# Performance work log

Measured on AMD Instinct MI355X. Metric: run time of the kernel, lower is better.

## Reference

```python
import jax, jax.numpy as jnp
import numpy as np

# Dims: B=batch, H=query heads, HKV=kv heads, T=query len, S=cache/key len, Dh=head dim
B, H, HKV, T, S, Dh = 2, 32, 8, 1024, 2048, 128
THRESH = 0.000488  # keep keys whose mean attention (over heads and queries) exceeds this


def setup_inputs() -> dict:
    key = jax.random.key(0)
    k1, k2, k3 = jax.random.split(key, 3)
    # attn_w emulates post-softmax attention probabilities: rows sum to 1 over key axis
    attn_w = jax.random.uniform(k1, (B, H, T, S), dtype=jnp.float32)
    attn_w = attn_w / attn_w.sum(axis=-1, keepdims=True)
    v = jax.random.normal(k2, (B, HKV, S, Dh), dtype=jnp.float32)
    w_o = jax.random.normal(k3, (H * Dh, H * Dh), dtype=jnp.float32) * 0.02  # o_proj weight (no bias, Mistral)
    return {"attn_w": attn_w, "v": v, "w_o": w_o}


def reference(attn_w, v, w_o):
    # keep = attn_w.mean(dim=(1,2)) > thresh  -> [B, S]
    keep = attn_w.mean(axis=(1, 2)) > THRESH
    pruned_weights = attn_w * keep[:, None, None, :].astype(attn_w.dtype)  # [B,H,T,S]
    # repeat_kv: [B,HKV,S,Dh] -> [B,H,S,Dh] via repeat_interleave on head axis
    groups = attn_w.shape[1] // v.shape[1]
    v_full = jnp.repeat(v, groups, axis=1)
    new_ctx = jnp.einsum('bhts,bhsd->bhtd', pruned_weights, v_full)  # [B,H,T,Dh]
    Bn, Hn, Tn, Dn = new_ctx.shape
    new_ctx = new_ctx.transpose(0, 2, 1, 3).reshape(Bn, Tn, Hn * Dn)  # [B,T,H*Dh]
    out = new_ctx @ w_o.T  # o_proj
    return (out, pruned_weights)
```

## Files before the change

kernel.cpp:

```cpp
#include <hip/hip_runtime.h>
#include <hip/hip_bf16.h>

#define B_ 2
#define H_ 32
#define HKV_ 8
#define T_ 1024
#define S_ 2048
#define DH_ 128
#define HD_ 4096
#define NROW_ 32768
#define THRESH_D 0.000488

typedef __attribute__((ext_vector_type(4))) float f32x4;
typedef __attribute__((ext_vector_type(8))) short bf16x8;

#define SCHED0() __builtin_amdgcn_sched_barrier(0)

__device__ __forceinline__ void gload_lds16(const void* g, void* l) {
  __builtin_amdgcn_global_load_lds(
      (const __attribute__((address_space(1))) void*)g,
      (__attribute__((address_space(3))) void*)l, 16, 0, 0);
}


__global__ void reduce_keep_k(const double* __restrict__ partial,
                              float* __restrict__ keep) {
  __shared__ double sh[4][64];
  int b = blockIdx.x >> 5;
  int s0 = (blockIdx.x & 31) * 64;
  int w = threadIdx.x >> 6, l = threadIdx.x & 63;
  const double* p = partial + (size_t)b * 256 * S_ + s0 + l;
  double sum = 0.0;
  #pragma unroll 8
  for (int y = 0; y < 64; ++y) sum += p[(size_t)(w * 64 + y) * S_];
  sh[w][l] = sum;
  __syncthreads();
  if (w == 0) {
    double t = (sh[0][l] + sh[1][l]) + (sh[2][l] + sh[3][l]);
    keep[b * S_ + s0 + l] = (t * (1.0 / 32768.0) > THRESH_D) ? 1.0f : 0.0f;
  }
}

__global__ void convert_wo_k(const float* __restrict__ w,
                             __hip_bfloat16* __restrict__ wb) {
  size_t idx = ((size_t)blockIdx.x * 256 + threadIdx.x) * 8;
  int n = (int)(idx >> 12);
  int k0 = (int)(idx & (HD_ - 1));
  float4 x = *(const float4*)(w + idx);
  float4 y = *(const float4*)(w + idx + 4);
  union { bf16x8 v8; __hip_bfloat16 h[8]; } u;
  u.h[0] = __float2bfloat16(x.x); u.h[1] = __float2bfloat16(x.y);
  u.h[2] = __float2bfloat16(x.z); u.h[3] = __float2bfloat16(x.w);
  u.h[4] = __float2bfloat16(y.x); u.h[5] = __float2bfloat16(y.y);
  u.h[6] = __float2bfloat16(y.z); u.h[7] = __float2bfloat16(y.w);
  int ksw = (k0 & ~63) | ((k0 ^ ((n & 7) << 3)) & 63);
  *(bf16x8*)(wb + (size_t)n * HD_ + ksw) = u.v8;
}

#define BK2 64
#define NS2 64

__global__ __launch_bounds__(512) void gemm2_k(
    const __hip_bfloat16* __restrict__ Actx,
    const __hip_bfloat16* __restrict__ Bw,
    float* __restrict__ out) {
  __shared__ __align__(16) __hip_bfloat16 As[2][128 * BK2];
  __shared__ __align__(16) __hip_bfloat16 Bs[2][128 * BK2];
  int tid = threadIdx.x;
  int lg = ((blockIdx.x & 7) << 6) | (blockIdx.x >> 3);
  int n0 = (lg >> 4) * 128;
  int m0 = (lg & 15) * 128;
  const __hip_bfloat16* Ap = Actx + (size_t)m0 * HD_;
  const __hip_bfloat16* Bp = Bw + (size_t)n0 * HD_;
  int wave = tid >> 6, lane = tid & 63;
  int l16 = lane & 15, lk = lane >> 4;

  f32x4 acc[8];
  f32x4 z = {0.f, 0.f, 0.f, 0.f};
  #pragma unroll
  for (int n = 0; n < 8; ++n) acc[n] = z;

  auto issue = [&](int ks, int buf) {
    const __hip_bfloat16* ga = Ap + (size_t)(tid >> 3) * HD_ + ks * BK2 + (tid & 7) * 8;
    const __hip_bfloat16* gb = Bp + (size_t)(tid >> 3) * HD_ + ks * BK2 + (tid & 7) * 8;
    char* la = (char*)&As[buf][0] + tid * 16;
    char* lb = (char*)&Bs[buf][0] + tid * 16;
    gload_lds16(ga, la);
    gload_lds16(ga + (size_t)64 * HD_, la + 8192);
    gload_lds16(gb, lb);
    gload_lds16(gb + (size_t)64 * HD_, lb + 8192);
  };

  auto mfmaStep = [&](int buf) {
    char* ab = (char*)&As[buf][0];
    char* bb = (char*)&Bs[buf][0];
    #pragma unroll
    for (int kk = 0; kk < 2; ++kk) {
      int kb = kk * 64 + lk * 16;
      int ar = wave * 16 + l16;
      bf16x8 af = *(const bf16x8*)(ab + (ar * 128 + (kb ^ ((ar & 7) << 4))));
      #pragma unroll
      for (int n = 0; n < 8; ++n) {
        int br = n * 16 + l16;
        bf16x8 bf = *(const bf16x8*)(bb + (br * 128 + (kb ^ ((br & 7) << 4))));
        acc[n] = __builtin_amdgcn_mfma_f32_16x16x32_bf16(af, bf, acc[n], 0, 0, 0);
      }
    }
  };

  issue(0, 0);
  for (int ks = 0; ks < NS2; ++ks) {
    int cur = ks & 1;
    if (ks + 1 < NS2) issue(ks + 1, cur ^ 1);
    SCHED0();
    if (ks + 1 < NS2) {
      asm volatile("s_waitcnt vmcnt(4) lgkmcnt(0)" ::: "memory");
    } else {
      asm volatile("s_waitcnt vmcnt(0) lgkmcnt(0)" ::: "memory");
    }
    SCHED0();
    __builtin_amdgcn_s_barrier();
    SCHED0();
    mfmaStep(cur);
    SCHED0();
    __builtin_amdgcn_s_barrier();
    SCHED0();
  }

  #pragma unroll
  for (int n = 0; n < 8; ++n)
    #pragma unroll
    for (int r = 0; r < 4; ++r) {
      int row = m0 + wave * 16 + lk * 4 + r;
      int col = n0 + n * 16 + l16;
      out[(size_t)row * HD_ + col] = acc[n][r];
    }
}


__global__ __launch_bounds__(256) void colsumA_k(
    const float* __restrict__ attn, double* __restrict__ partial,
    __hip_bfloat16* __restrict__ abf) {
  int tid = threadIdx.x;
  int b = blockIdx.z, y = blockIdx.y;
  int s = blockIdx.x * 1024 + tid * 4;
  const float* base = attn + (size_t)(b * NROW_ + y * 128) * S_ + s;
  __hip_bfloat16* ob = abf + (size_t)(b * NROW_ + y * 128) * S_;
  double a0 = 0.0, a1 = 0.0, a2 = 0.0, a3 = 0.0;
  #pragma unroll 2
  for (int r = 0; r < 128; ++r) {
    f32x4 vv = *(const f32x4*)(base + (size_t)r * S_);
    a0 += vv.x; a1 += vv.y; a2 += vv.z; a3 += vv.w;
    int ssw = (s & ~63) | ((s ^ ((r & 7) << 3)) & 63);
    union { ushort4 u4; __hip_bfloat16 h[4]; } u;
    u.h[0] = __float2bfloat16(vv.x); u.h[1] = __float2bfloat16(vv.y);
    u.h[2] = __float2bfloat16(vv.z); u.h[3] = __float2bfloat16(vv.w);
    *(ushort4*)(ob + (size_t)r * S_ + ssw) = u.u4;
  }
  double* o = partial + (size_t)(b * 256 + y) * S_ + s;
  o[0] = a0; o[1] = a1; o[2] = a2; o[3] = a3;
}

__global__ void convert_vA_k(const float* __restrict__ v,
                             const float* __restrict__ keep,
                             __hip_bfloat16* __restrict__ vt) {
  __shared__ float tile[32][33];
  int bh = blockIdx.z;
  int b = bh >> 3;
  int s0 = blockIdx.x * 32, d0 = blockIdx.y * 32;
  const float* vp = v + (size_t)bh * (S_ * DH_);
  __hip_bfloat16* vtp = vt + (size_t)bh * (S_ * DH_);
  int tx = threadIdx.x, ty = threadIdx.y;
  for (int i = 0; i < 32; i += 8)
    tile[ty + i][tx] = vp[(size_t)(s0 + ty + i) * DH_ + d0 + tx];
  __syncthreads();
  int s = s0 + tx;
  float kv = keep[b * S_ + s];
  for (int i = 0; i < 32; i += 8) {
    int d = d0 + ty + i;
    int ssw = (s & ~63) | ((s ^ ((d & 7) << 3)) & 63);
    vtp[(size_t)d * S_ + ssw] = __float2bfloat16(tile[tx][ty + i] * kv);
  }
}

#define BK1 64
#define NS1 32

__global__ __launch_bounds__(512, 4) void prune_gemm1A_k(
    const __hip_bfloat16* __restrict__ abf, const float* __restrict__ keep,
    const __hip_bfloat16* __restrict__ vt, float* __restrict__ pruned,
    __hip_bfloat16* __restrict__ ctx) {
  __shared__ __align__(16) __hip_bfloat16 As[2][128 * BK1];
  __shared__ __align__(16) __hip_bfloat16 Bs[2][128 * BK1];
  __shared__ __align__(16) float ksh[S_];

  int tid = threadIdx.x;
  int lg = ((blockIdx.x & 7) << 6) | (blockIdx.x >> 3);
  int bh = lg >> 3;
  int t0 = (lg & 7) * 128;
  int b = bh >> 5, h = bh & 31, hkv = h >> 2;
  int rot = (lg * 17) & 31;
  const __hip_bfloat16* Ab = abf + ((size_t)bh * T_ + t0) * S_;
  float* P = pruned + ((size_t)bh * T_ + t0) * S_;
  const __hip_bfloat16* Bv = vt + (size_t)(b * HKV_ + hkv) * (DH_ * S_);
  const float* kp = keep + b * S_;

  int wave = tid >> 6, lane = tid & 63;
  int l16 = lane & 15, lk = lane >> 4;

  f32x4 acc[8];
  f32x4 z = {0.f, 0.f, 0.f, 0.f};
  #pragma unroll
  for (int n = 0; n < 8; ++n) acc[n] = z;

  auto col = [&](int j) { return (j + rot) & 31; };

  auto issueA = [&](int cks, int buf) {
    const __hip_bfloat16* g0 = Ab + (size_t)(tid >> 3) * S_ + cks * BK1 + (tid & 7) * 8;
    char* la = (char*)&As[buf][0] + tid * 16;
    gload_lds16(g0, la);
    gload_lds16(g0 + (size_t)64 * S_, la + 8192);
  };

  auto issueB = [&](int cks, int buf) {
    const __hip_bfloat16* g0 = Bv + (size_t)(tid >> 3) * S_ + cks * BK1 + (tid & 7) * 8;
    char* lb = (char*)&Bs[buf][0] + tid * 16;
    gload_lds16(g0, lb);
    gload_lds16(g0 + (size_t)64 * S_, lb + 8192);
  };

  auto mfmaStep = [&](int buf) {
    char* ab = (char*)&As[buf][0];
    char* bb = (char*)&Bs[buf][0];
    #pragma unroll
    for (int kk = 0; kk < 2; ++kk) {
      int kb = kk * 64 + lk * 16;
      int ar = wave * 16 + l16;
      bf16x8 af = *(const bf16x8*)(ab + (ar * 128 + (kb ^ ((ar & 7) << 4))));
      #pragma unroll
      for (int n = 0; n < 8; ++n) {
        int br = n * 16 + l16;
        bf16x8 bf = *(const bf16x8*)(bb + (br * 128 + (kb ^ ((br & 7) << 4))));
        acc[n] = __builtin_amdgcn_mfma_f32_16x16x32_bf16(af, bf, acc[n], 0, 0, 0);
      }
    }
  };

  auto prunedWrite = [&](int cks, int buf) {
    char* ab = (char*)&As[buf][0];
    union { bf16x8 v; unsigned int d[4]; } u0, u1;
    u0.v = *(const bf16x8*)(ab + tid * 16);
    u1.v = *(const bf16x8*)(ab + tid * 16 + 8192);
    int row0 = tid >> 3;
    int scol = cks * BK1 + (((tid & 7) * 8) ^ ((row0 & 7) << 3));
    f32x4 k0 = *(const f32x4*)&ksh[scol];
    f32x4 k1 = *(const f32x4*)&ksh[scol + 4];
    f32x4 p00, p01, p10, p11;
    p00.x = __uint_as_float(u0.d[0] << 16) * k0.x;
    p00.y = __uint_as_float(u0.d[0] & 0xFFFF0000u) * k0.y;
    p00.z = __uint_as_float(u0.d[1] << 16) * k0.z;
    p00.w = __uint_as_float(u0.d[1] & 0xFFFF0000u) * k0.w;
    p01.x = __uint_as_float(u0.d[2] << 16) * k1.x;
    p01.y = __uint_as_float(u0.d[2] & 0xFFFF0000u) * k1.y;
    p01.z = __uint_as_float(u0.d[3] << 16) * k1.z;
    p01.w = __uint_as_float(u0.d[3] & 0xFFFF0000u) * k1.w;
    p10.x = __uint_as_float(u1.d[0] << 16) * k0.x;
    p10.y = __uint_as_float(u1.d[0] & 0xFFFF0000u) * k0.y;
    p10.z = __uint_as_float(u1.d[1] << 16) * k0.z;
    p10.w = __uint_as_float(u1.d[1] & 0xFFFF0000u) * k0.w;
    p11.x = __uint_as_float(u1.d[2] << 16) * k1.x;
    p11.y = __uint_as_float(u1.d[2] & 0xFFFF0000u) * k1.y;
    p11.z = __uint_as_float(u1.d[3] << 16) * k1.z;
    p11.w = __uint_as_float(u1.d[3] & 0xFFFF0000u) * k1.w;
    float* gp0 = P + (size_t)row0 * S_ + scol;
    float* gp1 = P + (size_t)(row0 + 64) * S_ + scol;
    *(f32x4*)gp0 = p00; *(f32x4*)(gp0 + 4) = p01;
    *(f32x4*)gp1 = p10; *(f32x4*)(gp1 + 4) = p11;
  };

  gload_lds16(kp + tid * 4, (char*)ksh + tid * 16);
  issueA(col(0), 0);
  issueB(col(0), 0);
  SCHED0();
  asm volatile("s_waitcnt vmcnt(4)" ::: "memory");
  SCHED0();
  __builtin_amdgcn_s_barrier();
  SCHED0();

  for (int ks = 0; ks < NS1; ++ks) {
    int cur = ks & 1;
    if (ks + 1 < NS1) {
      issueA(col(ks + 1), cur ^ 1);
      issueB(col(ks + 1), cur ^ 1);
    }
    SCHED0();
    if (ks == 0 || ks == NS1 - 1) {
      asm volatile("s_waitcnt vmcnt(4) lgkmcnt(0)" ::: "memory");
    } else {
      asm volatile("s_waitcnt vmcnt(8) lgkmcnt(0)" ::: "memory");
    }
    SCHED0();
    __builtin_amdgcn_s_barrier();
    SCHED0();
    mfmaStep(cur);
    prunedWrite(col(ks), cur);
    SCHED0();
    __builtin_amdgcn_s_barrier();
    SCHED0();
  }

  #pragma unroll
  for (int n = 0; n < 8; ++n)
    #pragma unroll
    for (int r = 0; r < 4; ++r) {
      int trow = t0 + wave * 16 + lk * 4 + r;
      int rowm = b * T_ + trow;
      int kcol = h * DH_ + n * 16 + l16;
      int ksw = (kcol & ~63) | ((kcol ^ ((rowm & 7) << 3)) & 63);
      ctx[(size_t)rowm * HD_ + ksw] = __float2bfloat16(acc[n][r]);
    }
}


__global__ __launch_bounds__(256) void colsumB_k(
    const float* __restrict__ attn, double* __restrict__ partial) {
  int tid = threadIdx.x;
  int b = blockIdx.z, y = blockIdx.y;
  int s = blockIdx.x * 1024 + tid * 4;
  const float* base = attn + (size_t)(b * NROW_ + y * 128) * S_ + s;
  double a0 = 0.0, a1 = 0.0, a2 = 0.0, a3 = 0.0;
  for (int r = 0; r < 128; ++r) {
    f32x4 vv = *(const f32x4*)(base + (size_t)r * S_);
    a0 += vv.x; a1 += vv.y; a2 += vv.z; a3 += vv.w;
  }
  double* o = partial + (size_t)(b * 256 + y) * S_ + s;
  o[0] = a0; o[1] = a1; o[2] = a2; o[3] = a3;
}

__global__ void convert_vB_k(const float* __restrict__ v,
                             __hip_bfloat16* __restrict__ vt) {
  __shared__ float tile[32][33];
  int bh = blockIdx.z;
  int s0 = blockIdx.x * 32, d0 = blockIdx.y * 32;
  const float* vp = v + (size_t)bh * (S_ * DH_);
  __hip_bfloat16* vtp = vt + (size_t)bh * (S_ * DH_);
  int tx = threadIdx.x, ty = threadIdx.y;
  for (int i = 0; i < 32; i += 8)
    tile[ty + i][tx] = vp[(size_t)(s0 + ty + i) * DH_ + d0 + tx];
  __syncthreads();
  int s = s0 + tx;
  for (int i = 0; i < 32; i += 8) {
    int d = d0 + ty + i;
    int ssw = (s & ~63) | ((s ^ ((d & 7) << 3)) & 63);
    vtp[(size_t)d * S_ + ssw] = __float2bfloat16(tile[tx][ty + i]);
  }
}

__global__ __launch_bounds__(512, 4) void prune_gemm1B_k(
    const float* __restrict__ attn, const float* __restrict__ keep,
    const __hip_bfloat16* __restrict__ vt, float* __restrict__ pruned,
    __hip_bfloat16* __restrict__ ctx) {
  __shared__ __align__(16) __hip_bfloat16 As[2][128 * BK1];
  __shared__ __align__(16) __hip_bfloat16 Bs[2][128 * BK1];
  __shared__ __align__(16) float ksh[S_];

  int tid = threadIdx.x;
  int lg = ((blockIdx.x & 7) << 6) | (blockIdx.x >> 3);
  int bh = lg >> 3;
  int t0 = (lg & 7) * 128;
  int b = bh >> 5, h = bh & 31, hkv = h >> 2;
  int rot = (lg * 17) & 31;
  const float* A = attn + ((size_t)bh * T_ + t0) * S_;
  float* P = pruned + ((size_t)bh * T_ + t0) * S_;
  const __hip_bfloat16* Bv = vt + (size_t)(b * HKV_ + hkv) * (DH_ * S_);
  const float* kp = keep + b * S_;

  int arow = tid >> 2;
  int acol = (tid & 3) * 16;
  int wave = tid >> 6, lane = tid & 63;
  int l16 = lane & 15, lk = lane >> 4;

  f32x4 acc[8];
  f32x4 z = {0.f, 0.f, 0.f, 0.f};
  #pragma unroll
  for (int n = 0; n < 8; ++n) acc[n] = z;

  f32x4 areg0[4], areg1[4];

  auto col = [&](int j) { return (j + rot) & 31; };

  auto issueA = [&](int cks, f32x4* bank) {
    const float* ga = A + (size_t)arow * S_ + cks * BK1 + acol;
    #pragma unroll
    for (int j = 0; j < 4; ++j) bank[j] = *(const f32x4*)(ga + j * 4);
  };

  auto issueB = [&](int cks, int buf) {
    const __hip_bfloat16* g0 = Bv + (size_t)(tid >> 3) * S_ + cks * BK1 + (tid & 7) * 8;
    char* lb = (char*)&Bs[buf][0] + tid * 16;
    gload_lds16(g0, lb);
    gload_lds16(g0 + (size_t)64 * S_, lb + 8192);
  };

  auto stageA = [&](int cks, int buf, const f32x4* bank) {
    f32x4 p[4];
    #pragma unroll
    for (int j = 0; j < 4; ++j) {
      f32x4 kv = *(const f32x4*)&ksh[cks * BK1 + acol + j * 4];
      p[j] = bank[j] * kv;
    }
    float* gp = P + (size_t)arow * S_ + cks * BK1 + acol;
    #pragma unroll
    for (int j = 0; j < 4; ++j) *(f32x4*)(gp + j * 4) = p[j];
    union { bf16x8 v8; __hip_bfloat16 h[8]; } u0, u1;
    const float* pf = (const float*)&p[0];
    #pragma unroll
    for (int j = 0; j < 8; ++j) u0.h[j] = __float2bfloat16(pf[j]);
    #pragma unroll
    for (int j = 0; j < 8; ++j) u1.h[j] = __float2bfloat16(pf[8 + j]);
    char* ab = (char*)&As[buf][0];
    int base0 = arow * 128 + acol * 2;
    int sw = (arow & 7) << 4;
    *(bf16x8*)(ab + (base0 ^ sw)) = u0.v8;
    *(bf16x8*)(ab + ((base0 + 16) ^ sw)) = u1.v8;
  };

  auto mfmaStep = [&](int buf) {
    char* ab = (char*)&As[buf][0];
    char* bb = (char*)&Bs[buf][0];
    #pragma unroll
    for (int kk = 0; kk < 2; ++kk) {
      int kb = kk * 64 + lk * 16;
      int ar = wave * 16 + l16;
      bf16x8 af = *(const bf16x8*)(ab + (ar * 128 + (kb ^ ((ar & 7) << 4))));
      #pragma unroll
      for (int n = 0; n < 8; ++n) {
        int br = n * 16 + l16;
        bf16x8 bf = *(const bf16x8*)(bb + (br * 128 + (kb ^ ((br & 7) << 4))));
        acc[n] = __builtin_amdgcn_mfma_f32_16x16x32_bf16(af, bf, acc[n], 0, 0, 0);
      }
    }
  };

  gload_lds16(kp + tid * 4, (char*)ksh + tid * 16);
  issueB(col(0), 0);
  issueA(col(0), areg0);
  SCHED0();
  asm volatile("s_waitcnt vmcnt(6)" ::: "memory");
  SCHED0();
  __builtin_amdgcn_s_barrier();
  SCHED0();
  issueA(col(1), areg1);
  stageA(col(0), 0, areg0);

  for (int ks = 0; ks < NS1; ks += 2) {
    {
      int cur = 0;
      if (ks + 1 < NS1) issueB(col(ks + 1), 1);
      if (ks + 2 < NS1) issueA(col(ks + 2), areg0);
      if (ks + 1 < NS1) stageA(col(ks + 1), 1, areg1);
      SCHED0();
      if (ks + 2 < NS1)      { asm volatile("s_waitcnt vmcnt(18) lgkmcnt(0)" ::: "memory"); }
      else if (ks + 1 < NS1) { asm volatile("s_waitcnt vmcnt(14) lgkmcnt(0)" ::: "memory"); }
      else                   { asm volatile("s_waitcnt vmcnt(4) lgkmcnt(0)" ::: "memory"); }
      SCHED0();
      __builtin_amdgcn_s_barrier();
      SCHED0();
      mfmaStep(cur);
      SCHED0();
      __builtin_amdgcn_s_barrier();
      SCHED0();
    }
    {
      int ko = ks + 1;
      int cur = 1;
      if (ko + 1 < NS1) issueB(col(ko + 1), 0);
      if (ko + 2 < NS1) issueA(col(ko + 2), areg1);
      if (ko + 1 < NS1) stageA(col(ko + 1), 0, areg0);
      SCHED0();
      if (ko + 2 < NS1)      { asm volatile("s_waitcnt vmcnt(18) lgkmcnt(0)" ::: "memory"); }
      else if (ko + 1 < NS1) { asm volatile("s_waitcnt vmcnt(14) lgkmcnt(0)" ::: "memory"); }
      else                   { asm volatile("s_waitcnt vmcnt(4) lgkmcnt(0)" ::: "memory"); }
      SCHED0();
      __builtin_amdgcn_s_barrier();
      SCHED0();
      mfmaStep(cur);
      SCHED0();
      __builtin_amdgcn_s_barrier();
      SCHED0();
    }
  }

  #pragma unroll
  for (int n = 0; n < 8; ++n)
    #pragma unroll
    for (int r = 0; r < 4; ++r) {
      int trow = t0 + wave * 16 + lk * 4 + r;
      int rowm = b * T_ + trow;
      int kcol = h * DH_ + n * 16 + l16;
      int ksw = (kcol & ~63) | ((kcol ^ ((rowm & 7) << 3)) & 63);
      ctx[(size_t)rowm * HD_ + ksw] = __float2bfloat16(acc[n][r]);
    }
}


extern "C" void kernel_launch(void* const* d_in, const int* in_sizes, int n_in,
                              void* d_out, int out_size, void* d_ws, size_t ws_size,
                              hipStream_t stream) {
  const float* attn = (const float*)d_in[0];
  const float* v = (const float*)d_in[1];
  const float* w_o = (const float*)d_in[2];
  float* out = (float*)d_out;
  float* pruned = out + (size_t)B_ * T_ * HD_;

  char* ws = (char*)d_ws;
  size_t off = 0;
  double* partial = (double*)(ws + off); off += (size_t)B_ * 256 * S_ * 8;
  float* keep = (float*)(ws + off);      off += (size_t)B_ * S_ * 4;
  __hip_bfloat16* vt = (__hip_bfloat16*)(ws + off);
  off += (size_t)B_ * HKV_ * DH_ * S_ * 2;
  __hip_bfloat16* wo = (__hip_bfloat16*)(ws + off);
  off += (size_t)HD_ * HD_ * 2;
  __hip_bfloat16* ctx = (__hip_bfloat16*)(ws + off);
  off += (size_t)B_ * T_ * HD_ * 2;
  __hip_bfloat16* abf = (__hip_bfloat16*)(ws + off);
  size_t need_abf = off + (size_t)B_ * NROW_ * S_ * 2;

  bool bigws = (ws_size >= need_abf);

  if (bigws) {
    colsumA_k<<<dim3(2, 256, B_), 256, 0, stream>>>(attn, partial, abf);
    reduce_keep_k<<<dim3(64), 256, 0, stream>>>(partial, keep);
    convert_vA_k<<<dim3(S_ / 32, DH_ / 32, B_ * HKV_), dim3(32, 8), 0, stream>>>(v, keep, vt);
    convert_wo_k<<<dim3((HD_ * HD_) / (256 * 8)), 256, 0, stream>>>(w_o, wo);
    prune_gemm1A_k<<<dim3(512), 512, 0, stream>>>(abf, keep, vt, pruned, ctx);
  } else {
    colsumB_k<<<dim3(2, 256, B_), 256, 0, stream>>>(attn, partial);
    reduce_keep_k<<<dim3(64), 256, 0, stream>>>(partial, keep);
    convert_vB_k<<<dim3(S_ / 32, DH_ / 32, B_ * HKV_), dim3(32, 8), 0, stream>>>(v, vt);
    convert_wo_k<<<dim3((HD_ * HD_) / (256 * 8)), 256, 0, stream>>>(w_o, wo);
    prune_gemm1B_k<<<dim3(512), 512, 0, stream>>>(attn, keep, vt, pruned, ctx);
  }
  gemm2_k<<<dim3(512), 512, 0, stream>>>(ctx, wo, out);

  (void)in_sizes; (void)n_in; (void)out_size; (void)ws_size;
}
```

Measured before the change: 454.2 us.

## Merge keep-reduction with w_o conversion and rotate colsum row order

Merges the keep-mask reduction and the w_o fp32-to-bf16 conversion into one kernel launch, with the first 64 blocks doing the reduction and the rest converting weights. This removes one launch and lets the two small jobs overlap. The column-sum kernels now start their 128-row loop at a per-block rotated offset, meant to spread concurrent reads across memory channels. In gemm1A the pruned-weight write is moved ahead of the MFMA step so its stores can overlap the math.

```diff
diff --git a/kernel.cpp b/kernel.cpp
--- a/kernel.cpp
+++ b/kernel.cpp
@@ -23,39 +23,41 @@
 }
 
 
-__global__ void reduce_keep_k(const double* __restrict__ partial,
-                              float* __restrict__ keep) {
+__global__ void reduce_wo_k(const double* __restrict__ partial,
+                            float* __restrict__ keep,
+                            const float* __restrict__ w,
+                            __hip_bfloat16* __restrict__ wb) {
   __shared__ double sh[4][64];
-  int b = blockIdx.x >> 5;
-  int s0 = (blockIdx.x & 31) * 64;
-  int w = threadIdx.x >> 6, l = threadIdx.x & 63;
-  const double* p = partial + (size_t)b * 256 * S_ + s0 + l;
-  double sum = 0.0;
-  #pragma unroll 8
-  for (int y = 0; y < 64; ++y) sum += p[(size_t)(w * 64 + y) * S_];
-  sh[w][l] = sum;
-  __syncthreads();
-  if (w == 0) {
-    double t = (sh[0][l] + sh[1][l]) + (sh[2][l] + sh[3][l]);
-    keep[b * S_ + s0 + l] = (t * (1.0 / 32768.0) > THRESH_D) ? 1.0f : 0.0f;
-  }
-}
-
-__global__ void convert_wo_k(const float* __restrict__ w,
-                             __hip_bfloat16* __restrict__ wb) {
-  size_t idx = ((size_t)blockIdx.x * 256 + threadIdx.x) * 8;
-  int n = (int)(idx >> 12);
-  int k0 = (int)(idx & (HD_ - 1));
-  float4 x = *(const float4*)(w + idx);
-  float4 y = *(const float4*)(w + idx + 4);
-  union { bf16x8 v8; __hip_bfloat16 h[8]; } u;
-  u.h[0] = __float2bfloat16(x.x); u.h[1] = __float2bfloat16(x.y);
-  u.h[2] = __float2bfloat16(x.z); u.h[3] = __float2bfloat16(x.w);
-  u.h[4] = __float2bfloat16(y.x); u.h[5] = __float2bfloat16(y.y);
-  u.h[6] = __float2bfloat16(y.z); u.h[7] = __float2bfloat16(y.w);
-  int ksw = (k0 & ~63) | ((k0 ^ ((n & 7) << 3)) & 63);
-  *(bf16x8*)(wb + (size_t)n * HD_ + ksw) = u.v8;
-}
+  if (blockIdx.x < 64) {
+    int b = blockIdx.x >> 5;
+    int s0 = (blockIdx.x & 31) * 64;
+    int wv = threadIdx.x >> 6, l = threadIdx.x & 63;
+    const double* p = partial + (size_t)b * 256 * S_ + s0 + l;
+    double sum = 0.0;
+    #pragma unroll 8
+    for (int y = 0; y < 64; ++y) sum += p[(size_t)(wv * 64 + y) * S_];
+    sh[wv][l] = sum;
+    __syncthreads();
+    if (wv == 0) {
+      double t = (sh[0][l] + sh[1][l]) + (sh[2][l] + sh[3][l]);
+      keep[b * S_ + s0 + l] = (t * (1.0 / 32768.0) > THRESH_D) ? 1.0f : 0.0f;
+    }
+  } else {
+    size_t idx = ((size_t)(blockIdx.x - 64) * 256 + threadIdx.x) * 8;
+    int n = (int)(idx >> 12);
+    int k0 = (int)(idx & (HD_ - 1));
+    float4 x = *(const float4*)(w + idx);
+    float4 y = *(const float4*)(w + idx + 4);
+    union { bf16x8 v8; __hip_bfloat16 h[8]; } u;
+    u.h[0] = __float2bfloat16(x.x); u.h[1] = __float2bfloat16(x.y);
+    u.h[2] = __float2bfloat16(x.z); u.h[3] = __float2bfloat16(x.w);
+    u.h[4] = __float2bfloat16(y.x); u.h[5] = __float2bfloat16(y.y);
+    u.h[6] = __float2bfloat16(y.z); u.h[7] = __float2bfloat16(y.w);
+    int ksw = (k0 & ~63) | ((k0 ^ ((n & 7) << 3)) & 63);
+    *(bf16x8*)(wb + (size_t)n * HD_ + ksw) = u.v8;
+  }
+}
+
 
 #define BK2 64
 #define NS2 64
@@ -146,9 +148,11 @@
   int s = blockIdx.x * 1024 + tid * 4;
   const float* base = attn + (size_t)(b * NROW_ + y * 128) * S_ + s;
   __hip_bfloat16* ob = abf + (size_t)(b * NROW_ + y * 128) * S_;
+  int rot = (y * 37 + b * 11 + blockIdx.x * 53) & 127;
   double a0 = 0.0, a1 = 0.0, a2 = 0.0, a3 = 0.0;
   #pragma unroll 2
-  for (int r = 0; r < 128; ++r) {
+  for (int i = 0; i < 128; ++i) {
+    int r = (i + rot) & 127;
     f32x4 vv = *(const f32x4*)(base + (size_t)r * S_);
     a0 += vv.x; a1 += vv.y; a2 += vv.z; a3 += vv.w;
     int ssw = (s & ~63) | ((s ^ ((r & 7) << 3)) & 63);
@@ -302,8 +306,8 @@
     SCHED0();
     __builtin_amdgcn_s_barrier();
     SCHED0();
+    prunedWrite(col(ks), cur);
     mfmaStep(cur);
-    prunedWrite(col(ks), cur);
     SCHED0();
     __builtin_amdgcn_s_barrier();
     SCHED0();
@@ -328,8 +332,11 @@
   int b = blockIdx.z, y = blockIdx.y;
   int s = blockIdx.x * 1024 + tid * 4;
   const float* base = attn + (size_t)(b * NROW_ + y * 128) * S_ + s;
+  int rot = (y * 37 + b * 11 + blockIdx.x * 53) & 127;
   double a0 = 0.0, a1 = 0.0, a2 = 0.0, a3 = 0.0;
-  for (int r = 0; r < 128; ++r) {
+  #pragma unroll 2
+  for (int i = 0; i < 128; ++i) {
+    int r = (i + rot) & 127;
     f32x4 vv = *(const f32x4*)(base + (size_t)r * S_);
     a0 += vv.x; a1 += vv.y; a2 += vv.z; a3 += vv.w;
   }
@@ -455,7 +462,6 @@
 
   for (int ks = 0; ks < NS1; ks += 2) {
     {
-      int cur = 0;
       if (ks + 1 < NS1) issueB(col(ks + 1), 1);
       if (ks + 2 < NS1) issueA(col(ks + 2), areg0);
       if (ks + 1 < NS1) stageA(col(ks + 1), 1, areg1);
@@ -466,14 +472,13 @@
       SCHED0();
       __builtin_amdgcn_s_barrier();
       SCHED0();
-      mfmaStep(cur);
+      mfmaStep(0);
       SCHED0();
       __builtin_amdgcn_s_barrier();
       SCHED0();
     }
     {
       int ko = ks + 1;
-      int cur = 1;
       if (ko + 1 < NS1) issueB(col(ko + 1), 0);
       if (ko + 2 < NS1) issueA(col(ko + 2), areg1);
       if (ko + 1 < NS1) stageA(col(ko + 1), 0, areg0);
@@ -484,7 +489,7 @@
       SCHED0();
       __builtin_amdgcn_s_barrier();
       SCHED0();
-      mfmaStep(cur);
+      mfmaStep(1);
       SCHED0();
       __builtin_amdgcn_s_barrier();
       SCHED0();
@@ -527,18 +532,17 @@
   size_t need_abf = off + (size_t)B_ * NROW_ * S_ * 2;
 
   bool bigws = (ws_size >= need_abf);
+  int wo_grid = 64 + (HD_ * HD_) / (256 * 8);
 
   if (bigws) {
     colsumA_k<<<dim3(2, 256, B_), 256, 0, stream>>>(attn, partial, abf);
-    reduce_keep_k<<<dim3(64), 256, 0, stream>>>(partial, keep);
+    reduce_wo_k<<<dim3(wo_grid), 256, 0, stream>>>(partial, keep, w_o, wo);
     convert_vA_k<<<dim3(S_ / 32, DH_ / 32, B_ * HKV_), dim3(32, 8), 0, stream>>>(v, keep, vt);
-    convert_wo_k<<<dim3((HD_ * HD_) / (256 * 8)), 256, 0, stream>>>(w_o, wo);
     prune_gemm1A_k<<<dim3(512), 512, 0, stream>>>(abf, keep, vt, pruned, ctx);
   } else {
     colsumB_k<<<dim3(2, 256, B_), 256, 0, stream>>>(attn, partial);
-    reduce_keep_k<<<dim3(64), 256, 0, stream>>>(partial, keep);
+    reduce_wo_k<<<dim3(wo_grid), 256, 0, stream>>>(partial, keep, w_o, wo);
     convert_vB_k<<<dim3(S_ / 32, DH_ / 32, B_ * HKV_), dim3(32, 8), 0, stream>>>(v, vt);
-    convert_wo_k<<<dim3((HD_ * HD_) / (256 * 8)), 256, 0, stream>>>(w_o, wo);
     prune_gemm1B_k<<<dim3(512), 512, 0, stream>>>(attn, keep, vt, pruned, ctx);
   }
   gemm2_k<<<dim3(512), 512, 0, stream>>>(ctx, wo, out);
```

Result: slower. 463.5 us (+2.0%).
